# Kernel tuning notes

Measured on AMD Instinct MI355X. Metric: run time of the kernel, lower is better.

Reference implementation:

```python
import jax, jax.numpy as jnp
import numpy as np

B, C, H, W = 2, 256, 64, 64
HEADS, DIM_HEAD = 8, 64
INNER = HEADS * DIM_HEAD


def setup_inputs() -> dict:
    key = jax.random.key(0)
    k1, k2, k3, k4 = jax.random.split(key, 4)
    x = jax.random.normal(k1, (B, C, H, W), dtype=jnp.float32)
    # 1x1 conv weights stored as [out_ch, in_ch]
    w_qkv = jax.random.normal(k2, (3 * INNER, C), dtype=jnp.float32) * (1.0 / np.sqrt(C))
    w_out = jax.random.normal(k3, (C, INNER), dtype=jnp.float32) * (1.0 / np.sqrt(INNER))
    b_out = jax.random.normal(k4, (C,), dtype=jnp.float32) * 0.01
    return {"x": x, "w_qkv": w_qkv, "w_out": w_out, "b_out": b_out}


def reference(x, w_qkv, w_out, b_out):
    b, c, h, w = x.shape
    n = h * w
    # 1x1 conv == channel matmul
    qkv = jnp.einsum('oc,bchw->bohw', w_qkv, x)  # [B, 3*inner, H, W]
    qkv = qkv.reshape(b, 3, HEADS, DIM_HEAD, n)
    qkv = jnp.transpose(qkv, (1, 0, 2, 4, 3))    # [3, B, heads, N, dim_head]
    q, k, v = qkv[0], qkv[1], qkv[2]
    scale = 1.0 / (DIM_HEAD ** 0.5)
    dots = jnp.einsum('bhnd,bhmd->bhnm', q, k) * scale  # [B, heads, N, N]
    attn = jax.nn.softmax(dots, axis=-1)
    out = jnp.einsum('bhnm,bhmd->bhnd', attn, v)        # [B, heads, N, dim_head]
    out = jnp.transpose(out, (0, 1, 3, 2)).reshape(b, INNER, h, w)
    return jnp.einsum('ci,bihw->bchw', w_out, out) + b_out[None, :, None, None]
```

## Files before the change

kernel.cpp:

```cpp
#include <hip/hip_runtime.h>
#include <hip/hip_bf16.h>

typedef unsigned short u16;
typedef __attribute__((ext_vector_type(8))) short bf16x8;
typedef __attribute__((ext_vector_type(4))) float f32x4;
typedef __attribute__((ext_vector_type(8))) unsigned short u16x8;
typedef __attribute__((ext_vector_type(4))) unsigned short u16x4;

#define N_POS 4096
#define HEADS 8
#define DHEAD 64
#define CIN   256
#define INNER 512
#define NSPLIT 4
#define JCHUNK (N_POS / NSPLIT)

__device__ __forceinline__ u16 f2bf(float f) {
    union { float f; unsigned int u; } v; v.f = f;
    unsigned int u = v.u + 0x7FFFu + ((v.u >> 16) & 1u);
    return (u16)(u >> 16);
}

__device__ __forceinline__ float b2f(u16 x) {
    union { float f; unsigned int u; } v;
    v.u = ((unsigned int)x) << 16;
    return v.f;
}

__device__ __forceinline__ unsigned int pkbf2(float lo, float hi) {
    union { __hip_bfloat162 b; unsigned int u; } cv;
    cv.b = __float22bfloat162_rn(make_float2(lo, hi));
    return cv.u;
}

__global__ __launch_bounds__(256) void k0_prep(const float* __restrict__ x,
                                               const float* __restrict__ w_qkv,
                                               const float* __restrict__ w_out,
                                               u16* __restrict__ xT,
                                               u16* __restrict__ wq,
                                               u16* __restrict__ wo) {
    int bid = blockIdx.x;
    int t   = threadIdx.x;
    if (bid < 256) {
        int b = bid >> 7, rest = bid & 127;
        int n  = (rest & 15) * 256 + t;
        int c0 = (rest >> 4) * 32;
        const float* xp = x + (size_t)b * CIN * N_POS + n;
        u16* op = xT + ((size_t)(b * N_POS + n)) * CIN + c0;
        for (int g = 0; g < 4; ++g) {
            u16x8 v;
            for (int j = 0; j < 8; ++j)
                v[j] = f2bf(xp[(size_t)(c0 + g * 8 + j) * N_POS]);
            *(u16x8*)(op + g * 8) = v;
        }
    } else if (bid < 448) {
        size_t idx = (size_t)(bid - 256) * 2048 + t * 8;
        u16x8 v;
        for (int j = 0; j < 8; ++j) v[j] = f2bf(w_qkv[idx + j]);
        *(u16x8*)(wq + idx) = v;
    } else {
        size_t idx = (size_t)(bid - 448) * 2048 + t * 8;
        u16x8 v;
        for (int j = 0; j < 8; ++j) v[j] = f2bf(w_out[idx + j]);
        *(u16x8*)(wo + idx) = v;
    }
}

__global__ __launch_bounds__(256, 4) void k1_qkv(const u16* __restrict__ wq,
                                                 const u16* __restrict__ xT,
                                                 u16* __restrict__ q_ws,
                                                 u16* __restrict__ k_ws,
                                                 u16* __restrict__ vt_ws) {
    __shared__ u16 Alds[64 * 40];
    __shared__ u16 Blds[128 * 40];
    int tid = threadIdx.x;
    int n0  = blockIdx.x * 128;
    int by  = blockIdx.y;
    int b   = blockIdx.z;
    int o0  = by * 64;
    int sel = by >> 3;
    int h   = by & 7;
    int wv = tid >> 6, l = tid & 63, quad = l >> 4, l15 = l & 15;
    int srow = tid >> 2, sseg = tid & 3;
    int brow = tid >> 1, bseg = tid & 1;

    f32x4 acc[8] = {};
    for (int c0 = 0; c0 < CIN; c0 += 32) {
        *(u16x8*)&Alds[srow * 40 + sseg * 8] =
            *(const u16x8*)(wq + (size_t)(o0 + srow) * CIN + c0 + sseg * 8);
        const u16* xp = xT + ((size_t)(b * N_POS + n0 + brow)) * CIN + c0 + bseg * 16;
        *(u16x8*)&Blds[brow * 40 + bseg * 16]     = *(const u16x8*)xp;
        *(u16x8*)&Blds[brow * 40 + bseg * 16 + 8] = *(const u16x8*)(xp + 8);
        __syncthreads();
        bf16x8 af = *(const bf16x8*)&Alds[(wv * 16 + l15) * 40 + quad * 8];
        for (int nt = 0; nt < 8; ++nt) {
            bf16x8 bfrag = *(const bf16x8*)&Blds[(nt * 16 + l15) * 40 + quad * 8];
            acc[nt] = __builtin_amdgcn_mfma_f32_16x16x32_bf16(af, bfrag, acc[nt], 0, 0, 0);
        }
        __syncthreads();
    }
    const float QSCALE = 0.125f * 1.44269504088896f;
    float sc = (sel == 0) ? QSCALE : 1.0f;
    int dbase = wv * 16 + quad * 4;
    for (int nt = 0; nt < 8; ++nt) {
        int n = n0 + nt * 16 + l15;
        if (sel < 2) {
            u16* base = (sel == 0) ? q_ws : k_ws;
            u16x4 pk;
            for (int r = 0; r < 4; ++r) pk[r] = f2bf(acc[nt][r] * sc);
            *(u16x4*)&base[((size_t)((b * HEADS + h) * N_POS + n)) * DHEAD + dbase] = pk;
        } else {
            for (int r = 0; r < 4; ++r)
                vt_ws[((size_t)((b * HEADS + h) * DHEAD + dbase + r)) * N_POS + n] =
                    f2bf(acc[nt][r]);
        }
    }
}

__global__ __launch_bounds__(256, 4) void k2_attn(const u16* __restrict__ q_ws,
                                                  const u16* __restrict__ k_ws,
                                                  const u16* __restrict__ vt_ws,
                                                  u16* __restrict__ op_ws,
                                                  float* __restrict__ lw_ws) {
    __shared__ u16 Klds[64 * 72];
    __shared__ u16 Vlds[64 * 72];
    int tid = threadIdx.x;
    int q0  = blockIdx.x * 128;
    int bh  = blockIdx.y;
    int half = blockIdx.z;
    int jbase = half * JCHUNK;
    int wv = tid >> 6, l = tid & 63, quad = l >> 4, l15 = l & 15;
    int srow = tid >> 2, sseg = tid & 3;
    int srowp = (srow & 0x23) | ((srow & 4) << 2) | ((srow & 0x18) >> 1);

    const u16* qp = q_ws + ((size_t)(bh * N_POS + q0 + wv * 32 + l15)) * DHEAD + quad * 8;
    bf16x8 bq[2][2];
    for (int it = 0; it < 2; ++it) {
        bq[it][0] = *(const bf16x8*)(qp + (size_t)it * 16 * DHEAD);
        bq[it][1] = *(const bf16x8*)(qp + (size_t)it * 16 * DHEAD + 32);
    }

    f32x4 Oacc[2][4] = {};
    float lsum[2] = {0.f, 0.f};

    const u16* kp = k_ws + ((size_t)(bh * N_POS + srow)) * DHEAD + sseg * 16;
    const u16* vp = vt_ws + ((size_t)(bh * DHEAD + srow)) * N_POS + sseg * 16;

    u16x8 pf0 = *(const u16x8*)(kp + (size_t)jbase * DHEAD);
    u16x8 pf1 = *(const u16x8*)(kp + (size_t)jbase * DHEAD + 8);
    u16x8 pf2 = *(const u16x8*)(vp + jbase);
    u16x8 pf3 = *(const u16x8*)(vp + jbase + 8);

    for (int j0 = jbase; j0 < jbase + JCHUNK; j0 += 64) {
        *(u16x8*)&Klds[srowp * 72 + sseg * 16]     = pf0;
        *(u16x8*)&Klds[srowp * 72 + sseg * 16 + 8] = pf1;
        *(u16x8*)&Vlds[srow * 72 + sseg * 16]      = pf2;
        *(u16x8*)&Vlds[srow * 72 + sseg * 16 + 8]  = pf3;
        __syncthreads();

        if (j0 + 64 < jbase + JCHUNK) {
            const u16* kpj = kp + (size_t)(j0 + 64) * DHEAD;
            pf0 = *(const u16x8*)kpj;
            pf1 = *(const u16x8*)(kpj + 8);
            pf2 = *(const u16x8*)(vp + j0 + 64);
            pf3 = *(const u16x8*)(vp + j0 + 72);
        }

        unsigned int pkw[2][2][4];
        for (int p = 0; p < 2; ++p)
            for (int a = 0; a < 2; ++a) {
                const u16* kb = &Klds[((2 * p + a) * 16 + l15) * 72 + quad * 8];
                bf16x8 kf0 = *(const bf16x8*)kb;
                bf16x8 kf1 = *(const bf16x8*)(kb + 32);
                f32x4 z[2];
                for (int it = 0; it < 2; ++it) {
                    f32x4 t = {};
                    t = __builtin_amdgcn_mfma_f32_16x16x32_bf16(kf0, bq[it][0], t, 0, 0, 0);
                    t = __builtin_amdgcn_mfma_f32_16x16x32_bf16(kf1, bq[it][1], t, 0, 0, 0);
                    z[it] = t;
                }
                for (int it = 0; it < 2; ++it) {
                    float e0 = __builtin_amdgcn_exp2f(z[it][0]);
                    float e1 = __builtin_amdgcn_exp2f(z[it][1]);
                    float e2 = __builtin_amdgcn_exp2f(z[it][2]);
                    float e3 = __builtin_amdgcn_exp2f(z[it][3]);
                    lsum[it] += (e0 + e1) + (e2 + e3);
                    pkw[it][p][2 * a]     = pkbf2(e0, e1);
                    pkw[it][p][2 * a + 1] = pkbf2(e2, e3);
                }
            }

        for (int dt = 0; dt < 4; ++dt)
            for (int p = 0; p < 2; ++p) {
                bf16x8 vf = *(const bf16x8*)&Vlds[(dt * 16 + l15) * 72 + p * 32 + quad * 8];
                for (int it = 0; it < 2; ++it) {
                    union { unsigned int u[4]; bf16x8 v; } cv;
                    cv.u[0] = pkw[it][p][0]; cv.u[1] = pkw[it][p][1];
                    cv.u[2] = pkw[it][p][2]; cv.u[3] = pkw[it][p][3];
                    Oacc[it][dt] = __builtin_amdgcn_mfma_f32_16x16x32_bf16(vf, cv.v, Oacc[it][dt], 0, 0, 0);
                }
            }
        __syncthreads();
    }

    int b = bh >> 3, h = bh & 7;
    u16* opb   = op_ws + (size_t)half * 2 * N_POS * INNER;
    float* lwb = lw_ws + (size_t)half * 2 * HEADS * N_POS;
    for (int it = 0; it < 2; ++it) {
        float ls = lsum[it];
        ls += __shfl_xor(ls, 16);
        ls += __shfl_xor(ls, 32);
        int n = q0 + wv * 32 + it * 16 + l15;
        if (quad == 0) lwb[(size_t)bh * N_POS + n] = ls;
        u16* dst = opb + ((size_t)(b * N_POS + n)) * INNER + h * DHEAD;
        for (int dt = 0; dt < 4; ++dt) {
            u16x4 w;
            for (int r = 0; r < 4; ++r) w[r] = f2bf(Oacc[it][dt][r]);
            *(u16x4*)&dst[dt * 16 + quad * 4] = w;
        }
    }
}

__global__ __launch_bounds__(256) void k3_out(const u16* __restrict__ wo,
                                              const float* __restrict__ b_out,
                                              const u16* __restrict__ op_ws,
                                              const float* __restrict__ lw_ws,
                                              float* __restrict__ out) {
    __shared__ u16 Alds[64 * 40];
    __shared__ u16 Blds[64 * 40];
    int tid = threadIdx.x;
    int n0 = blockIdx.x * 64;
    int c0 = blockIdx.y * 64;
    int b  = blockIdx.z;
    int wv = tid >> 6, l = tid & 63, quad = l >> 4, l15 = l & 15;
    int srow = tid >> 2, sseg = tid & 3;

    f32x4 acc[4] = {};
    for (int i0 = 0; i0 < INNER; i0 += 32) {
        *(u16x8*)&Alds[srow * 40 + sseg * 8] =
            *(const u16x8*)(wo + (size_t)(c0 + srow) * INNER + i0 + sseg * 8);
        {
            int i = i0 + sseg * 8;
            int h = i >> 6;
            int n = n0 + srow;
            size_t lidx = ((size_t)(b * HEADS + h)) * N_POS + n;
            float ls = 0.f;
            for (int s = 0; s < NSPLIT; ++s)
                ls += lw_ws[(size_t)s * 2 * HEADS * N_POS + lidx];
            float inv = 1.0f / ls;
            const u16* p = op_ws + ((size_t)(b * N_POS + n)) * INNER + i;
            float a8[8] = {};
            for (int s = 0; s < NSPLIT; ++s) {
                u16x8 v = *(const u16x8*)(p + (size_t)s * 2 * N_POS * INNER);
                for (int k = 0; k < 8; ++k) a8[k] += b2f(v[k]);
            }
            u16x8 o;
            for (int k = 0; k < 8; ++k) o[k] = f2bf(a8[k] * inv);
            *(u16x8*)&Blds[srow * 40 + sseg * 8] = o;
        }
        __syncthreads();
        bf16x8 af = *(const bf16x8*)&Alds[(wv * 16 + l15) * 40 + quad * 8];
        for (int nt = 0; nt < 4; ++nt) {
            bf16x8 bfrag = *(const bf16x8*)&Blds[(nt * 16 + l15) * 40 + quad * 8];
            acc[nt] = __builtin_amdgcn_mfma_f32_16x16x32_bf16(af, bfrag, acc[nt], 0, 0, 0);
        }
        __syncthreads();
    }
    for (int r = 0; r < 4; ++r) {
        int c = c0 + wv * 16 + quad * 4 + r;
        float bias = b_out[c];
        for (int nt = 0; nt < 4; ++nt) {
            int n = n0 + nt * 16 + l15;
            out[((size_t)(b * CIN + c)) * N_POS + n] = acc[nt][r] + bias;
        }
    }
}

extern "C" void kernel_launch(void* const* d_in, const int* in_sizes, int n_in,
                              void* d_out, int out_size, void* d_ws, size_t ws_size,
                              hipStream_t stream) {
    const float* x     = (const float*)d_in[0];
    const float* w_qkv = (const float*)d_in[1];
    const float* w_out = (const float*)d_in[2];
    const float* b_out = (const float*)d_in[3];
    float* out = (float*)d_out;

    u16* ws    = (u16*)d_ws;
    u16* xT    = ws;
    u16* q_ws  = xT   + (size_t)2 * N_POS * CIN;
    u16* k_ws  = q_ws + (size_t)2 * HEADS * N_POS * DHEAD;
    u16* vt_ws = k_ws + (size_t)2 * HEADS * N_POS * DHEAD;
    u16* wq_bf = vt_ws + (size_t)2 * HEADS * N_POS * DHEAD;
    u16* wo_bf = wq_bf + (size_t)3 * INNER * CIN;
    u16* op_ws = wo_bf + (size_t)CIN * INNER;
    float* lw_ws = (float*)(op_ws + (size_t)NSPLIT * 2 * N_POS * INNER);

    hipLaunchKernelGGL(k0_prep, dim3(512), dim3(256), 0, stream,
                       x, w_qkv, w_out, xT, wq_bf, wo_bf);
    hipLaunchKernelGGL(k1_qkv, dim3(32, 24, 2), dim3(256), 0, stream,
                       wq_bf, xT, q_ws, k_ws, vt_ws);
    hipLaunchKernelGGL(k2_attn, dim3(32, 16, NSPLIT), dim3(256), 0, stream,
                       q_ws, k_ws, vt_ws, op_ws, lw_ws);
    hipLaunchKernelGGL(k3_out, dim3(64, 4, 2), dim3(256), 0, stream,
                       wo_bf, b_out, op_ws, lw_ws, out);
}
```

Measured before the change: 190.4 us.

## Halve attention key splits and deepen K-tiles in QKV and output GEMMs

Reduces the attention key-split count from 4 to 2, which halves the partial outputs written and then re-read and merged in the output projection. Widens the K-step of the QKV projection from 32 to 64 and of the output projection from 32 to 128, so each iteration loads more per sync and issues more MFMAs between barriers. In exchange, the attention kernel has fewer blocks to keep the GPU busy, and the larger LDS tiles in the output kernel lower occupancy (launch bound set to 2 blocks).

```diff
diff --git a/kernel.cpp b/kernel.cpp
--- a/kernel.cpp
+++ b/kernel.cpp
@@ -12,7 +12,7 @@
 #define DHEAD 64
 #define CIN   256
 #define INNER 512
-#define NSPLIT 4
+#define NSPLIT 2
 #define JCHUNK (N_POS / NSPLIT)
 
 __device__ __forceinline__ u16 f2bf(float f) {
@@ -71,8 +71,8 @@
                                                  u16* __restrict__ q_ws,
                                                  u16* __restrict__ k_ws,
                                                  u16* __restrict__ vt_ws) {
-    __shared__ u16 Alds[64 * 40];
-    __shared__ u16 Blds[128 * 40];
+    __shared__ u16 Alds[64 * 72];
+    __shared__ u16 Blds[128 * 72];
     int tid = threadIdx.x;
     int n0  = blockIdx.x * 128;
     int by  = blockIdx.y;
@@ -81,21 +81,24 @@
     int sel = by >> 3;
     int h   = by & 7;
     int wv = tid >> 6, l = tid & 63, quad = l >> 4, l15 = l & 15;
-    int srow = tid >> 2, sseg = tid & 3;
-    int brow = tid >> 1, bseg = tid & 1;
+    int arow = tid >> 2, aseg = (tid & 3) * 16;
+    int brow = tid >> 1, bseg = (tid & 1) * 32;
 
     f32x4 acc[8] = {};
-    for (int c0 = 0; c0 < CIN; c0 += 32) {
-        *(u16x8*)&Alds[srow * 40 + sseg * 8] =
-            *(const u16x8*)(wq + (size_t)(o0 + srow) * CIN + c0 + sseg * 8);
-        const u16* xp = xT + ((size_t)(b * N_POS + n0 + brow)) * CIN + c0 + bseg * 16;
-        *(u16x8*)&Blds[brow * 40 + bseg * 16]     = *(const u16x8*)xp;
-        *(u16x8*)&Blds[brow * 40 + bseg * 16 + 8] = *(const u16x8*)(xp + 8);
-        __syncthreads();
-        bf16x8 af = *(const bf16x8*)&Alds[(wv * 16 + l15) * 40 + quad * 8];
+    for (int c0 = 0; c0 < CIN; c0 += 64) {
+        const u16* wp = wq + (size_t)(o0 + arow) * CIN + c0 + aseg;
+        *(u16x8*)&Alds[arow * 72 + aseg]     = *(const u16x8*)wp;
+        *(u16x8*)&Alds[arow * 72 + aseg + 8] = *(const u16x8*)(wp + 8);
+        const u16* xp = xT + ((size_t)(b * N_POS + n0 + brow)) * CIN + c0 + bseg;
+        for (int g = 0; g < 4; ++g)
+            *(u16x8*)&Blds[brow * 72 + bseg + g * 8] = *(const u16x8*)(xp + g * 8);
+        __syncthreads();
+        bf16x8 af0 = *(const bf16x8*)&Alds[(wv * 16 + l15) * 72 + quad * 8];
+        bf16x8 af1 = *(const bf16x8*)&Alds[(wv * 16 + l15) * 72 + 32 + quad * 8];
         for (int nt = 0; nt < 8; ++nt) {
-            bf16x8 bfrag = *(const bf16x8*)&Blds[(nt * 16 + l15) * 40 + quad * 8];
-            acc[nt] = __builtin_amdgcn_mfma_f32_16x16x32_bf16(af, bfrag, acc[nt], 0, 0, 0);
+            const u16* bb = &Blds[(nt * 16 + l15) * 72 + quad * 8];
+            acc[nt] = __builtin_amdgcn_mfma_f32_16x16x32_bf16(af0, *(const bf16x8*)bb, acc[nt], 0, 0, 0);
+            acc[nt] = __builtin_amdgcn_mfma_f32_16x16x32_bf16(af1, *(const bf16x8*)(bb + 32), acc[nt], 0, 0, 0);
         }
         __syncthreads();
     }
@@ -221,26 +224,27 @@
     }
 }
 
-__global__ __launch_bounds__(256) void k3_out(const u16* __restrict__ wo,
-                                              const float* __restrict__ b_out,
-                                              const u16* __restrict__ op_ws,
-                                              const float* __restrict__ lw_ws,
-                                              float* __restrict__ out) {
-    __shared__ u16 Alds[64 * 40];
-    __shared__ u16 Blds[64 * 40];
+__global__ __launch_bounds__(256, 2) void k3_out(const u16* __restrict__ wo,
+                                                 const float* __restrict__ b_out,
+                                                 const u16* __restrict__ op_ws,
+                                                 const float* __restrict__ lw_ws,
+                                                 float* __restrict__ out) {
+    __shared__ u16 Alds[64 * 136];
+    __shared__ u16 Blds[64 * 136];
     int tid = threadIdx.x;
     int n0 = blockIdx.x * 64;
     int c0 = blockIdx.y * 64;
     int b  = blockIdx.z;
     int wv = tid >> 6, l = tid & 63, quad = l >> 4, l15 = l & 15;
-    int srow = tid >> 2, sseg = tid & 3;
+    int srow = tid >> 2, sseg = (tid & 3) * 32;
 
     f32x4 acc[4] = {};
-    for (int i0 = 0; i0 < INNER; i0 += 32) {
-        *(u16x8*)&Alds[srow * 40 + sseg * 8] =
-            *(const u16x8*)(wo + (size_t)(c0 + srow) * INNER + i0 + sseg * 8);
+    for (int i0 = 0; i0 < INNER; i0 += 128) {
+        const u16* wp = wo + (size_t)(c0 + srow) * INNER + i0 + sseg;
+        for (int g = 0; g < 4; ++g)
+            *(u16x8*)&Alds[srow * 136 + sseg + g * 8] = *(const u16x8*)(wp + g * 8);
         {
-            int i = i0 + sseg * 8;
+            int i = i0 + sseg;
             int h = i >> 6;
             int n = n0 + srow;
             size_t lidx = ((size_t)(b * HEADS + h)) * N_POS + n;
@@ -249,20 +253,24 @@
                 ls += lw_ws[(size_t)s * 2 * HEADS * N_POS + lidx];
             float inv = 1.0f / ls;
             const u16* p = op_ws + ((size_t)(b * N_POS + n)) * INNER + i;
-            float a8[8] = {};
-            for (int s = 0; s < NSPLIT; ++s) {
-                u16x8 v = *(const u16x8*)(p + (size_t)s * 2 * N_POS * INNER);
-                for (int k = 0; k < 8; ++k) a8[k] += b2f(v[k]);
+            for (int g = 0; g < 4; ++g) {
+                float a8[8] = {};
+                for (int s = 0; s < NSPLIT; ++s) {
+                    u16x8 v = *(const u16x8*)(p + (size_t)s * 2 * N_POS * INNER + g * 8);
+                    for (int k = 0; k < 8; ++k) a8[k] += b2f(v[k]);
+                }
+                u16x8 o;
+                for (int k = 0; k < 8; ++k) o[k] = f2bf(a8[k] * inv);
+                *(u16x8*)&Blds[srow * 136 + sseg + g * 8] = o;
             }
-            u16x8 o;
-            for (int k = 0; k < 8; ++k) o[k] = f2bf(a8[k] * inv);
-            *(u16x8*)&Blds[srow * 40 + sseg * 8] = o;
-        }
-        __syncthreads();
-        bf16x8 af = *(const bf16x8*)&Alds[(wv * 16 + l15) * 40 + quad * 8];
-        for (int nt = 0; nt < 4; ++nt) {
-            bf16x8 bfrag = *(const bf16x8*)&Blds[(nt * 16 + l15) * 40 + quad * 8];
-            acc[nt] = __builtin_amdgcn_mfma_f32_16x16x32_bf16(af, bfrag, acc[nt], 0, 0, 0);
+        }
+        __syncthreads();
+        for (int kc = 0; kc < 4; ++kc) {
+            bf16x8 af = *(const bf16x8*)&Alds[(wv * 16 + l15) * 136 + kc * 32 + quad * 8];
+            for (int nt = 0; nt < 4; ++nt) {
+                bf16x8 bfrag = *(const bf16x8*)&Blds[(nt * 16 + l15) * 136 + kc * 32 + quad * 8];
+                acc[nt] = __builtin_amdgcn_mfma_f32_16x16x32_bf16(af, bfrag, acc[nt], 0, 0, 0);
+            }
         }
         __syncthreads();
     }
```

After: 178.7 us. 6.1% less time.
